# Kernel optimization log

Measured on AMD Instinct MI355X. Metric: run time of the kernel, lower is better.

## Reference

```python
import jax, jax.numpy as jnp
import numpy as np

ATT = 32      # att_size per spatial dim (pooled grid is 32x32, N=1024)
HEADS = 8

def _pool_sum(x, out):
    # adaptive max + adaptive avg pool (exact uniform windows since W%out==0)
    B, C, W, H = x.shape
    kw, kh = W // out, H // out
    r = x.reshape(B, C, out, kw, out, kh)
    return r.max(axis=(3, 5)) + r.mean(axis=(3, 5))

def _lerp_axis(x, out_len, axis):
    in_len = x.shape[axis]
    pos = jnp.arange(out_len, dtype=x.dtype) * ((in_len - 1) / (out_len - 1))
    i0 = jnp.floor(pos).astype(jnp.int32)
    i1 = jnp.minimum(i0 + 1, in_len - 1)
    t = pos - i0.astype(x.dtype)
    shp = [1] * x.ndim
    shp[axis] = out_len
    t = t.reshape(shp)
    return jnp.take(x, i0, axis=axis) * (1 - t) + jnp.take(x, i1, axis=axis) * t

def _upsample_bilinear_ac(x, out_h, out_w):
    # bilinear, align_corners=True (separable)
    return _lerp_axis(_lerp_axis(x, out_h, 2), out_w, 3)

def setup_inputs() -> dict:
    key = jax.random.key(0)
    k1, k2, k3, k4 = jax.random.split(key, 4)
    B, C, W, H = 8, 256, 128, 128
    input1 = jax.random.normal(k1, (B, C, W, H), dtype=jnp.float32)
    input2 = jax.random.normal(k2, (B, C // 2, W, H), dtype=jnp.float32)
    # 1x1 conv: out=C, in=C//2 (kaiming-ish scale)
    conv_w = jax.random.normal(k3, (C, C // 2), dtype=jnp.float32) * (1.0 / np.sqrt(C // 2))
    conv_b = jax.random.normal(k4, (C,), dtype=jnp.float32) * 0.01
    return {"input1": input1, "input2": input2, "conv_w": conv_w, "conv_b": conv_b}

def reference(input1, input2, conv_w, conv_b):
    B, C, W, H = input1.shape
    # channel projection (1x1 conv) since input2 has C//2 channels
    x2 = jnp.einsum('bihw,oi->bohw', input2, conv_w) + conv_b[None, :, None, None]
    p1 = _pool_sum(input1, ATT)   # [B,C,32,32]
    p2 = _pool_sum(x2, ATT)
    N = ATT * ATT
    q = p1.reshape(B, C, N).transpose(2, 0, 1)  # [N,B,C]
    k = p2.reshape(B, C, N).transpose(2, 0, 1)
    v = k
    scale = 1.0 / np.sqrt(C // HEADS)
    w = jnp.einsum('nbc,nec->nbe', q, k)        # [N,B,B]
    w = jax.nn.softmax(w * scale, axis=-1)
    a = jnp.einsum('nbe,nec->nbc', w, v)        # [N,B,C]
    attn = a.transpose(1, 2, 0).reshape(B, C, ATT, ATT)
    up = _upsample_bilinear_ac(attn, W, H)
    return jax.nn.sigmoid(up)
```

## Files before the change

kernel.cpp:

```cpp
#include <hip/hip_runtime.h>
#include <math.h>

namespace {

constexpr int Bn = 8, Cn = 256, CIN = 128, Wd = 128, Hd = 128, ATTn = 32, Nn = ATTn * ATTn;

typedef __attribute__((ext_vector_type(8))) short short8;
typedef __attribute__((ext_vector_type(4))) float f32x4;

__device__ inline unsigned short bf16_rne(float f) {
    unsigned int u = __float_as_uint(f);
    unsigned int r = (u + 0x7FFFu + ((u >> 16) & 1u)) >> 16;
    return (unsigned short)r;
}

__global__ __launch_bounds__(512) void front_kernel(const float* __restrict__ in1,
                                                    const float* __restrict__ in2,
                                                    const float* __restrict__ cw,
                                                    const float* __restrict__ cb,
                                                    float* __restrict__ p1t,
                                                    float* __restrict__ p2t) {
    __shared__ __align__(16) unsigned char sIn[2][16384];

    const int t = threadIdx.x;
    const int bid = blockIdx.x;

    if (bid >= 512) {
        const int bid2 = bid - 512;
        const int b = bid2 >> 5, oy = bid2 & 31;
        const int c = t & 255, xh = t >> 8;
        const float* src = in1 + (((size_t)(b * Cn + c) * Wd + oy * 4)) * Hd + xh * 64;
        float mx[16], sm[16];
#pragma unroll
        for (int q = 0; q < 16; ++q) { mx[q] = -INFINITY; sm[q] = 0.f; }
#pragma unroll
        for (int dy = 0; dy < 4; ++dy) {
            const float4* rp = reinterpret_cast<const float4*>(src + dy * Hd);
#pragma unroll
            for (int q = 0; q < 16; ++q) {
                float4 v = rp[q];
                mx[q] = fmaxf(mx[q], fmaxf(fmaxf(v.x, v.y), fmaxf(v.z, v.w)));
                sm[q] += (v.x + v.y) + (v.z + v.w);
            }
        }
        float* dst = p1t + ((size_t)b * Nn + oy * 32 + xh * 16) * Cn + c;
#pragma unroll
        for (int q = 0; q < 16; ++q)
            dst[(size_t)q * Cn] = mx[q] + sm[q] * (1.f / 16.f);
        return;
    }

    const int w = t >> 6;
    const int l = t & 63;
    const int b = bid >> 6;
    const int oy = (bid >> 1) & 31;
    const int half = bid & 1;

    const int n_lo = l & 15;
    const int khi = l >> 4;

    short8 bfrag[2][4];
#pragma unroll
    for (int f = 0; f < 2; ++f) {
        const int n = w * 32 + f * 16 + n_lo;
#pragma unroll
        for (int kk = 0; kk < 4; ++kk) {
            const float* wp = cw + n * CIN + kk * 32 + khi * 8;
            float4 va = *reinterpret_cast<const float4*>(wp);
            float4 vb = *reinterpret_cast<const float4*>(wp + 4);
            short8 s;
            s[0] = (short)bf16_rne(va.x); s[1] = (short)bf16_rne(va.y);
            s[2] = (short)bf16_rne(va.z); s[3] = (short)bf16_rne(va.w);
            s[4] = (short)bf16_rne(vb.x); s[5] = (short)bf16_rne(vb.y);
            s[6] = (short)bf16_rne(vb.z); s[7] = (short)bf16_rne(vb.w);
            bfrag[f][kk] = s;
        }
    }
    const float bias2_0 = 2.f * cb[w * 32 + n_lo];
    const float bias2_1 = 2.f * cb[w * 32 + 16 + n_lo];

    const int xq = t & 3, dy = (t >> 2) & 3, k4 = t >> 4;
    const int row = oy * 4 + dy;
    const float* src = in2 + (((size_t)(b * CIN + k4 * 4)) * Wd + row) * Hd + half * 64 + xq * 4;

    float4 r0, r1, r2, r3;
#define STAGE_LOAD(g)                                                   \
    {   const float* p_ = src + (g) * 16;                               \
        r0 = *reinterpret_cast<const float4*>(p_);                      \
        r1 = *reinterpret_cast<const float4*>(p_ + Wd * Hd);            \
        r2 = *reinterpret_cast<const float4*>(p_ + 2 * Wd * Hd);        \
        r3 = *reinterpret_cast<const float4*>(p_ + 3 * Wd * Hd); }

#define WRQ(buf, dx, c0, c1, c2, c3)                                    \
    {   const int px_ = dy * 4 + (dx);                                  \
        uint2 u_;                                                       \
        u_.x = (unsigned int)bf16_rne(c0) | ((unsigned int)bf16_rne(c1) << 16); \
        u_.y = (unsigned int)bf16_rne(c2) | ((unsigned int)bf16_rne(c3) << 16); \
        const int off_ = (xq * 4096 + px_ * 256 + k4 * 8) ^ (((px_ & 7) << 4) ^ ((xq & 3) << 5)); \
        *reinterpret_cast<uint2*>(&sIn[buf][off_]) = u_; }

#define STAGE_WRITE(buf)                                                \
    {   WRQ(buf, 0, r0.x, r1.x, r2.x, r3.x)                             \
        WRQ(buf, 1, r0.y, r1.y, r2.y, r3.y)                             \
        WRQ(buf, 2, r0.z, r1.z, r2.z, r3.z)                             \
        WRQ(buf, 3, r0.w, r1.w, r2.w, r3.w) }

    STAGE_LOAD(0)
    STAGE_WRITE(0)
    __syncthreads();

    const int px = n_lo;
    for (int g = 0; g < 4; ++g) {
        const int buf = g & 1;
        if (g < 3) STAGE_LOAD(g + 1)

        const unsigned char* base = sIn[buf];
#pragma unroll
        for (int c = 0; c < 4; ++c) {
            const int swz = ((px & 7) << 4) ^ ((c & 3) << 5);
            f32x4 acc0 = {0.f, 0.f, 0.f, 0.f};
            f32x4 acc1 = {0.f, 0.f, 0.f, 0.f};
#pragma unroll
            for (int kk = 0; kk < 4; ++kk) {
                short8 a = *reinterpret_cast<const short8*>(
                    base + ((c * 4096 + px * 256 + kk * 64 + khi * 16) ^ swz));
                acc0 = __builtin_amdgcn_mfma_f32_16x16x32_bf16(a, bfrag[0][kk], acc0, 0, 0, 0);
                acc1 = __builtin_amdgcn_mfma_f32_16x16x32_bf16(a, bfrag[1][kk], acc1, 0, 0, 0);
            }
            float mx0 = fmaxf(fmaxf(acc0[0], acc0[1]), fmaxf(acc0[2], acc0[3]));
            float sm0 = (acc0[0] + acc0[1]) + (acc0[2] + acc0[3]);
            float mx1 = fmaxf(fmaxf(acc1[0], acc1[1]), fmaxf(acc1[2], acc1[3]));
            float sm1 = (acc1[0] + acc1[1]) + (acc1[2] + acc1[3]);
            mx0 = fmaxf(mx0, __shfl_xor(mx0, 16)); sm0 += __shfl_xor(sm0, 16);
            mx0 = fmaxf(mx0, __shfl_xor(mx0, 32)); sm0 += __shfl_xor(sm0, 32);
            mx1 = fmaxf(mx1, __shfl_xor(mx1, 16)); sm1 += __shfl_xor(sm1, 16);
            mx1 = fmaxf(mx1, __shfl_xor(mx1, 32)); sm1 += __shfl_xor(sm1, 32);
            if (l < 16) {
                const int cell = oy * 32 + half * 16 + g * 4 + c;
                float* dst = p2t + ((size_t)b * Nn + cell) * Cn + w * 32 + n_lo;
                dst[0]  = mx0 + sm0 * (1.f / 16.f) + bias2_0;
                dst[16] = mx1 + sm1 * (1.f / 16.f) + bias2_1;
            }
        }

        if (g < 3) STAGE_WRITE((g + 1) & 1)
        __syncthreads();
    }
#undef STAGE_LOAD
#undef STAGE_WRITE
#undef WRQ
}

__global__ __launch_bounds__(256) void attn_kernel(const float* __restrict__ p1t,
                                                   const float* __restrict__ p2t,
                                                   float* __restrict__ att) {
    __shared__ float q[Bn][260];
    __shared__ float kk[Bn][260];
    __shared__ float wsm[Bn][8];
    const int n = blockIdx.x, t = threadIdx.x;

#pragma unroll
    for (int i = 0; i < 2; ++i) {
        const int f = t + i * 256;
        const int bb = f >> 6, cq = f & 63;
        const size_t off = ((size_t)bb * Nn + n) * Cn + cq * 4;
        *reinterpret_cast<float4*>(&q[bb][cq * 4])  = *reinterpret_cast<const float4*>(p1t + off);
        *reinterpret_cast<float4*>(&kk[bb][cq * 4]) = *reinterpret_cast<const float4*>(p2t + off);
    }
    __syncthreads();

    {
        const int chunk = t & 3, pair = t >> 2;
        const int e = pair & 7, bb = pair >> 3;
        float s = 0.f;
#pragma unroll
        for (int i = 0; i < 64; ++i)
            s = fmaf(q[bb][i * 4 + chunk], kk[e][i * 4 + chunk], s);
        s += __shfl_xor(s, 1);
        s += __shfl_xor(s, 2);
        s *= 0.17677669529663687f;
        float m = fmaxf(s, __shfl_xor(s, 4));
        m = fmaxf(m, __shfl_xor(m, 8));
        m = fmaxf(m, __shfl_xor(m, 16));
        float p = __expf(s - m);
        float d = p + __shfl_xor(p, 4);
        d += __shfl_xor(d, 8);
        d += __shfl_xor(d, 16);
        if (chunk == 0) wsm[bb][e] = p / d;
    }
    __syncthreads();

    float kv[8];
#pragma unroll
    for (int e = 0; e < 8; ++e) kv[e] = kk[e][t];
#pragma unroll
    for (int bb = 0; bb < 8; ++bb) {
        float s = 0.f;
#pragma unroll
        for (int e = 0; e < 8; ++e) s = fmaf(wsm[bb][e], kv[e], s);
        att[((size_t)bb * Cn + t) * Nn + n] = s;
    }
}

__global__ __launch_bounds__(256) void upsample_kernel(const float* __restrict__ att,
                                                       float* __restrict__ out) {
    __shared__ float tile[ATTn * ATTn];
    int bc = blockIdx.x, t = threadIdx.x;
    reinterpret_cast<float4*>(tile)[t] =
        reinterpret_cast<const float4*>(att + (size_t)bc * Nn)[t];
    __syncthreads();

    int tx = t & 31, ty = t >> 5;
    int xi0[4], xi1[4];
    float xt[4];
#pragma unroll
    for (int j = 0; j < 4; ++j) {
        int x = tx * 4 + j;
        float pos = (float)x * (31.f / 127.f);
        int i0 = (int)pos;
        xi0[j] = i0;
        xi1[j] = min(i0 + 1, 31);
        xt[j] = pos - (float)i0;
    }

    for (int r = 0; r < 16; ++r) {
        int y = ty + r * 8;
        float posy = (float)y * (31.f / 127.f);
        int y0 = (int)posy;
        int y1 = min(y0 + 1, 31);
        float ft = posy - (float)y0;
        float o_[4];
#pragma unroll
        for (int j = 0; j < 4; ++j) {
            float v00 = tile[y0 * 32 + xi0[j]];
            float v01 = tile[y0 * 32 + xi1[j]];
            float v10 = tile[y1 * 32 + xi0[j]];
            float v11 = tile[y1 * 32 + xi1[j]];
            float top = v00 * (1.f - ft) + v10 * ft;
            float bot = v01 * (1.f - ft) + v11 * ft;
            float val = top * (1.f - xt[j]) + bot * xt[j];
            o_[j] = 1.f / (1.f + __expf(-val));
        }
        *reinterpret_cast<float4*>(out + ((size_t)bc * Wd + y) * Hd + tx * 4) =
            make_float4(o_[0], o_[1], o_[2], o_[3]);
    }
}

}

extern "C" void kernel_launch(void* const* d_in, const int* in_sizes, int n_in,
                              void* d_out, int out_size, void* d_ws, size_t ws_size,
                              hipStream_t stream) {
    const float* input1 = (const float*)d_in[0];
    const float* input2 = (const float*)d_in[1];
    const float* conv_w = (const float*)d_in[2];
    const float* conv_b = (const float*)d_in[3];
    float* out = (float*)d_out;

    float* p1t = (float*)d_ws;
    float* p2t = p1t + (size_t)Bn * Cn * Nn;
    float* att = p2t + (size_t)Bn * Cn * Nn;

    front_kernel<<<dim3(768), dim3(512), 0, stream>>>(input1, input2, conv_w, conv_b, p1t, p2t);
    attn_kernel<<<dim3(Nn), dim3(256), 0, stream>>>(p1t, p2t, att);
    upsample_kernel<<<dim3(Bn * Cn), dim3(256), 0, stream>>>(att, out);
}
```

Before: 120.6 us.

## Restructure front kernel: coalesced input1 pooling via LDS transpose, single-stage conv tiles

The input1 pooling blocks are rewritten so that each wave reads full contiguous rows per channel, reduces across lanes, and transposes through shared memory before writing channel-contiguous output. Previously each thread walked its own channel with strided float4 loads. The conv-pooling blocks now handle a quarter row each (1280 blocks total) and issue all global loads up front in a single stage with a new swizzle, replacing the double-buffered 4-stage loop. Launch bounds are raised to 4 blocks per CU for occupancy. The trade-off is more register pressure and no overlap of load with compute inside a block.

```diff
diff --git a/kernel.cpp b/kernel.cpp
--- a/kernel.cpp
+++ b/kernel.cpp
@@ -14,51 +14,69 @@
     return (unsigned short)r;
 }
 
-__global__ __launch_bounds__(512) void front_kernel(const float* __restrict__ in1,
-                                                    const float* __restrict__ in2,
-                                                    const float* __restrict__ cw,
-                                                    const float* __restrict__ cb,
-                                                    float* __restrict__ p1t,
-                                                    float* __restrict__ p2t) {
-    __shared__ __align__(16) unsigned char sIn[2][16384];
+__device__ inline int fsw(int px) { return (px ^ (px >> 3)) & 7; }
+
+__global__ __launch_bounds__(512, 4) void front_kernel(const float* __restrict__ in1,
+                                                       const float* __restrict__ in2,
+                                                       const float* __restrict__ cw,
+                                                       const float* __restrict__ cb,
+                                                       float* __restrict__ p1t,
+                                                       float* __restrict__ p2t) {
+    __shared__ __align__(16) unsigned char smem[33792];
 
     const int t = threadIdx.x;
     const int bid = blockIdx.x;
-
-    if (bid >= 512) {
-        const int bid2 = bid - 512;
-        const int b = bid2 >> 5, oy = bid2 & 31;
-        const int c = t & 255, xh = t >> 8;
-        const float* src = in1 + (((size_t)(b * Cn + c) * Wd + oy * 4)) * Hd + xh * 64;
-        float mx[16], sm[16];
-#pragma unroll
-        for (int q = 0; q < 16; ++q) { mx[q] = -INFINITY; sm[q] = 0.f; }
-#pragma unroll
-        for (int dy = 0; dy < 4; ++dy) {
-            const float4* rp = reinterpret_cast<const float4*>(src + dy * Hd);
-#pragma unroll
-            for (int q = 0; q < 16; ++q) {
-                float4 v = rp[q];
-                mx[q] = fmaxf(mx[q], fmaxf(fmaxf(v.x, v.y), fmaxf(v.z, v.w)));
-                sm[q] += (v.x + v.y) + (v.z + v.w);
-            }
-        }
-        float* dst = p1t + ((size_t)b * Nn + oy * 32 + xh * 16) * Cn + c;
-#pragma unroll
-        for (int q = 0; q < 16; ++q)
-            dst[(size_t)q * Cn] = mx[q] + sm[q] * (1.f / 16.f);
-        return;
-    }
-
     const int w = t >> 6;
     const int l = t & 63;
-    const int b = bid >> 6;
-    const int oy = (bid >> 1) & 31;
-    const int half = bid & 1;
+
+    if (bid < 256) {
+        const int b = bid >> 5, oy = bid & 31;
+        float* tile = reinterpret_cast<float*>(smem) + w * 1056;
+        const int x4 = l & 31, dyp = l >> 5;
+        const float* base = in1 + ((size_t)(b * Cn + w * 32) * Wd + oy * 4 + dyp) * Hd + x4 * 4;
+#pragma unroll 4
+        for (int ch = 0; ch < 32; ++ch) {
+            const float* p = base + (size_t)ch * Wd * Hd;
+            f32x4 v0 = *reinterpret_cast<const f32x4*>(p);
+            f32x4 v1 = *reinterpret_cast<const f32x4*>(p + 2 * Hd);
+            float mx = fmaxf(fmaxf(fmaxf(v0[0], v0[1]), fmaxf(v0[2], v0[3])),
+                             fmaxf(fmaxf(v1[0], v1[1]), fmaxf(v1[2], v1[3])));
+            float sm = ((v0[0] + v0[1]) + (v0[2] + v0[3])) +
+                       ((v1[0] + v1[1]) + (v1[2] + v1[3]));
+            mx = fmaxf(mx, __shfl_xor(mx, 32));
+            sm += __shfl_xor(sm, 32);
+            if (l < 32) tile[x4 * 33 + ch] = mx + sm * (1.f / 16.f);
+        }
+        const int cl = l & 31, oxp = l >> 5;
+#pragma unroll
+        for (int it = 0; it < 16; ++it) {
+            const int ox = it * 2 + oxp;
+            const float v = tile[ox * 33 + cl];
+            p1t[((size_t)b * Nn + oy * 32 + ox) * Cn + w * 32 + cl] = v;
+        }
+        return;
+    }
+
+    const int bid2 = bid - 256;
+    const int b = bid2 >> 7;
+    const int r = bid2 & 127;
+    const int oy = r >> 2, xq = r & 3;
+
+    f32x4 ra[2][4];
+    int x4v[2], rowv[2], k4v[2];
+#pragma unroll
+    for (int h = 0; h < 2; ++h) {
+        const int i = t + h * 512;
+        x4v[h] = i & 7; rowv[h] = (i >> 3) & 3; k4v[h] = i >> 5;
+        const float* p = in2 + ((size_t)(b * CIN + k4v[h] * 4) * Wd + oy * 4 + rowv[h]) * Hd
+                         + xq * 32 + x4v[h] * 4;
+#pragma unroll
+        for (int kk2 = 0; kk2 < 4; ++kk2)
+            ra[h][kk2] = *reinterpret_cast<const f32x4*>(p + (size_t)kk2 * Wd * Hd);
+    }
 
     const int n_lo = l & 15;
     const int khi = l >> 4;
-
     short8 bfrag[2][4];
 #pragma unroll
     for (int f = 0; f < 2; ++f) {
@@ -66,89 +84,61 @@
 #pragma unroll
         for (int kk = 0; kk < 4; ++kk) {
             const float* wp = cw + n * CIN + kk * 32 + khi * 8;
-            float4 va = *reinterpret_cast<const float4*>(wp);
-            float4 vb = *reinterpret_cast<const float4*>(wp + 4);
+            f32x4 va = *reinterpret_cast<const f32x4*>(wp);
+            f32x4 vb = *reinterpret_cast<const f32x4*>(wp + 4);
             short8 s;
-            s[0] = (short)bf16_rne(va.x); s[1] = (short)bf16_rne(va.y);
-            s[2] = (short)bf16_rne(va.z); s[3] = (short)bf16_rne(va.w);
-            s[4] = (short)bf16_rne(vb.x); s[5] = (short)bf16_rne(vb.y);
-            s[6] = (short)bf16_rne(vb.z); s[7] = (short)bf16_rne(vb.w);
+            s[0] = (short)bf16_rne(va[0]); s[1] = (short)bf16_rne(va[1]);
+            s[2] = (short)bf16_rne(va[2]); s[3] = (short)bf16_rne(va[3]);
+            s[4] = (short)bf16_rne(vb[0]); s[5] = (short)bf16_rne(vb[1]);
+            s[6] = (short)bf16_rne(vb[2]); s[7] = (short)bf16_rne(vb[3]);
             bfrag[f][kk] = s;
         }
     }
     const float bias2_0 = 2.f * cb[w * 32 + n_lo];
     const float bias2_1 = 2.f * cb[w * 32 + 16 + n_lo];
 
-    const int xq = t & 3, dy = (t >> 2) & 3, k4 = t >> 4;
-    const int row = oy * 4 + dy;
-    const float* src = in2 + (((size_t)(b * CIN + k4 * 4)) * Wd + row) * Hd + half * 64 + xq * 4;
-
-    float4 r0, r1, r2, r3;
-#define STAGE_LOAD(g)                                                   \
-    {   const float* p_ = src + (g) * 16;                               \
-        r0 = *reinterpret_cast<const float4*>(p_);                      \
-        r1 = *reinterpret_cast<const float4*>(p_ + Wd * Hd);            \
-        r2 = *reinterpret_cast<const float4*>(p_ + 2 * Wd * Hd);        \
-        r3 = *reinterpret_cast<const float4*>(p_ + 3 * Wd * Hd); }
-
-#define WRQ(buf, dx, c0, c1, c2, c3)                                    \
-    {   const int px_ = dy * 4 + (dx);                                  \
-        uint2 u_;                                                       \
-        u_.x = (unsigned int)bf16_rne(c0) | ((unsigned int)bf16_rne(c1) << 16); \
-        u_.y = (unsigned int)bf16_rne(c2) | ((unsigned int)bf16_rne(c3) << 16); \
-        const int off_ = (xq * 4096 + px_ * 256 + k4 * 8) ^ (((px_ & 7) << 4) ^ ((xq & 3) << 5)); \
-        *reinterpret_cast<uint2*>(&sIn[buf][off_]) = u_; }
-
-#define STAGE_WRITE(buf)                                                \
-    {   WRQ(buf, 0, r0.x, r1.x, r2.x, r3.x)                             \
-        WRQ(buf, 1, r0.y, r1.y, r2.y, r3.y)                             \
-        WRQ(buf, 2, r0.z, r1.z, r2.z, r3.z)                             \
-        WRQ(buf, 3, r0.w, r1.w, r2.w, r3.w) }
-
-    STAGE_LOAD(0)
-    STAGE_WRITE(0)
-    __syncthreads();
-
-    const int px = n_lo;
-    for (int g = 0; g < 4; ++g) {
-        const int buf = g & 1;
-        if (g < 3) STAGE_LOAD(g + 1)
-
-        const unsigned char* base = sIn[buf];
-#pragma unroll
-        for (int c = 0; c < 4; ++c) {
-            const int swz = ((px & 7) << 4) ^ ((c & 3) << 5);
-            f32x4 acc0 = {0.f, 0.f, 0.f, 0.f};
-            f32x4 acc1 = {0.f, 0.f, 0.f, 0.f};
-#pragma unroll
-            for (int kk = 0; kk < 4; ++kk) {
-                short8 a = *reinterpret_cast<const short8*>(
-                    base + ((c * 4096 + px * 256 + kk * 64 + khi * 16) ^ swz));
-                acc0 = __builtin_amdgcn_mfma_f32_16x16x32_bf16(a, bfrag[0][kk], acc0, 0, 0, 0);
-                acc1 = __builtin_amdgcn_mfma_f32_16x16x32_bf16(a, bfrag[1][kk], acc1, 0, 0, 0);
-            }
-            float mx0 = fmaxf(fmaxf(acc0[0], acc0[1]), fmaxf(acc0[2], acc0[3]));
-            float sm0 = (acc0[0] + acc0[1]) + (acc0[2] + acc0[3]);
-            float mx1 = fmaxf(fmaxf(acc1[0], acc1[1]), fmaxf(acc1[2], acc1[3]));
-            float sm1 = (acc1[0] + acc1[1]) + (acc1[2] + acc1[3]);
-            mx0 = fmaxf(mx0, __shfl_xor(mx0, 16)); sm0 += __shfl_xor(sm0, 16);
-            mx0 = fmaxf(mx0, __shfl_xor(mx0, 32)); sm0 += __shfl_xor(sm0, 32);
-            mx1 = fmaxf(mx1, __shfl_xor(mx1, 16)); sm1 += __shfl_xor(sm1, 16);
-            mx1 = fmaxf(mx1, __shfl_xor(mx1, 32)); sm1 += __shfl_xor(sm1, 32);
-            if (l < 16) {
-                const int cell = oy * 32 + half * 16 + g * 4 + c;
-                float* dst = p2t + ((size_t)b * Nn + cell) * Cn + w * 32 + n_lo;
-                dst[0]  = mx0 + sm0 * (1.f / 16.f) + bias2_0;
-                dst[16] = mx1 + sm1 * (1.f / 16.f) + bias2_1;
-            }
-        }
-
-        if (g < 3) STAGE_WRITE((g + 1) & 1)
-        __syncthreads();
-    }
-#undef STAGE_LOAD
-#undef STAGE_WRITE
-#undef WRQ
+#pragma unroll
+    for (int h = 0; h < 2; ++h) {
+#pragma unroll
+        for (int j = 0; j < 4; ++j) {
+            const int px = x4v[h] * 16 + rowv[h] * 4 + j;
+            uint2 u;
+            u.x = (unsigned int)bf16_rne(ra[h][0][j]) | ((unsigned int)bf16_rne(ra[h][1][j]) << 16);
+            u.y = (unsigned int)bf16_rne(ra[h][2][j]) | ((unsigned int)bf16_rne(ra[h][3][j]) << 16);
+            const int off = px * 256 + ((k4v[h] * 8) ^ (fsw(px) << 4));
+            *reinterpret_cast<uint2*>(smem + off) = u;
+        }
+    }
+    __syncthreads();
+
+#pragma unroll
+    for (int cl = 0; cl < 8; ++cl) {
+        f32x4 acc0 = {0.f, 0.f, 0.f, 0.f};
+        f32x4 acc1 = {0.f, 0.f, 0.f, 0.f};
+        const int px = cl * 16 + n_lo;
+        const int sw = fsw(px) << 4;
+#pragma unroll
+        for (int kk = 0; kk < 4; ++kk) {
+            short8 a = *reinterpret_cast<const short8*>(
+                smem + px * 256 + ((kk * 64 + khi * 16) ^ sw));
+            acc0 = __builtin_amdgcn_mfma_f32_16x16x32_bf16(a, bfrag[0][kk], acc0, 0, 0, 0);
+            acc1 = __builtin_amdgcn_mfma_f32_16x16x32_bf16(a, bfrag[1][kk], acc1, 0, 0, 0);
+        }
+        float mx0 = fmaxf(fmaxf(acc0[0], acc0[1]), fmaxf(acc0[2], acc0[3]));
+        float sm0 = (acc0[0] + acc0[1]) + (acc0[2] + acc0[3]);
+        float mx1 = fmaxf(fmaxf(acc1[0], acc1[1]), fmaxf(acc1[2], acc1[3]));
+        float sm1 = (acc1[0] + acc1[1]) + (acc1[2] + acc1[3]);
+        mx0 = fmaxf(mx0, __shfl_xor(mx0, 16)); sm0 += __shfl_xor(sm0, 16);
+        mx0 = fmaxf(mx0, __shfl_xor(mx0, 32)); sm0 += __shfl_xor(sm0, 32);
+        mx1 = fmaxf(mx1, __shfl_xor(mx1, 16)); sm1 += __shfl_xor(sm1, 16);
+        mx1 = fmaxf(mx1, __shfl_xor(mx1, 32)); sm1 += __shfl_xor(sm1, 32);
+        if (l < 16) {
+            const int cell = oy * 32 + xq * 8 + cl;
+            float* dst = p2t + ((size_t)b * Nn + cell) * Cn + w * 32 + n_lo;
+            dst[0]  = mx0 + sm0 * (1.f / 16.f) + bias2_0;
+            dst[16] = mx1 + sm1 * (1.f / 16.f) + bias2_1;
+        }
+    }
 }
 
 __global__ __launch_bounds__(256) void attn_kernel(const float* __restrict__ p1t,
@@ -261,7 +251,7 @@
     float* p2t = p1t + (size_t)Bn * Cn * Nn;
     float* att = p2t + (size_t)Bn * Cn * Nn;
 
-    front_kernel<<<dim3(768), dim3(512), 0, stream>>>(input1, input2, conv_w, conv_b, p1t, p2t);
+    front_kernel<<<dim3(1280), dim3(512), 0, stream>>>(input1, input2, conv_w, conv_b, p1t, p2t);
     attn_kernel<<<dim3(Nn), dim3(256), 0, stream>>>(p1t, p2t, att);
     upsample_kernel<<<dim3(Bn * Cn), dim3(256), 0, stream>>>(att, out);
 }
```

Result: faster. 110.8 us (-8.1%).
